# Kernel tuning notes

Hardware: AMD Instinct MI355X
Metric: run time of the kernel (lower is better)

Reference implementation:

```python
import jax, jax.numpy as jnp
import numpy as np

DIM = 1024
HEADS = 16

def setup_inputs() -> dict:
    key = jax.random.key(0)
    ks = jax.random.split(key, 5)
    x = jax.random.normal(ks[0], (4, 2048, DIM), dtype=jnp.float32)
    s = 1.0 / np.sqrt(DIM)
    Wqkv = jax.random.normal(ks[1], (DIM, 3 * DIM), dtype=jnp.float32) * s
    bqkv = jnp.zeros((3 * DIM,), dtype=jnp.float32)
    Wproj = jax.random.normal(ks[2], (DIM, DIM), dtype=jnp.float32) * s
    bproj = jnp.zeros((DIM,), dtype=jnp.float32)
    return {"x": x, "Wqkv": Wqkv, "bqkv": bqkv, "Wproj": Wproj, "bproj": bproj}

def reference(x, Wqkv, bqkv, Wproj, bproj):
    B, N, D = x.shape
    H = HEADS
    hd = D // H
    scale = hd ** (-0.5)
    qkv = x @ Wqkv + bqkv                      # [B, N, 3D]
    q, k, v = jnp.split(qkv, 3, axis=-1)
    # [B, N, H, hd] -> [B, H, N, hd]
    q = q.reshape(B, N, H, hd).transpose(0, 2, 1, 3)
    k = k.reshape(B, N, H, hd).transpose(0, 2, 1, 3)
    v = v.reshape(B, N, H, hd).transpose(0, 2, 1, 3)
    attn = jnp.einsum('bhqd,bhkd->bhqk', q, k) * scale
    attn = jax.nn.softmax(attn, axis=-1)
    out = jnp.einsum('bhqk,bhkd->bhqd', attn, v)
    out = out.transpose(0, 2, 1, 3).reshape(B, N, D)
    return out @ Wproj + bproj
```

## Files before the change

### kernel.cpp

```cpp
#include <hip/hip_runtime.h>
#include <hip/hip_bf16.h>
#include <math.h>


typedef __bf16 bf16;
typedef __bf16 bf16x4 __attribute__((ext_vector_type(4)));
typedef __bf16 bf16x8 __attribute__((ext_vector_type(8)));
typedef float f32x4 __attribute__((ext_vector_type(4)));

#define AS1(p) ((const __attribute__((address_space(1))) void*)(p))
#define AS3(p) ((__attribute__((address_space(3))) void*)(p))

__device__ __forceinline__ void async16(const void* g, void* l) {
    __builtin_amdgcn_global_load_lds(AS1(g), AS3(l), 16, 0, 0);
}

#if __has_builtin(__builtin_amdgcn_exp2f)
#define EXP2(x) __builtin_amdgcn_exp2f(x)
#else
#define EXP2(x) exp2f(x)
#endif

#define QSCALE 0.18033688011112042f


__global__ void cvt_f32_bf16(const float* __restrict__ in, bf16* __restrict__ out, int n4) {
    int i = blockIdx.x * blockDim.x + threadIdx.x;
    if (i < n4) {
        float4 v = ((const float4*)in)[i];
        bf16x4 o;
        o.x = (bf16)v.x; o.y = (bf16)v.y; o.z = (bf16)v.z; o.w = (bf16)v.w;
        ((bf16x4*)out)[i] = o;
    }
}

__global__ void transpose_cvt(const float* __restrict__ in, bf16* __restrict__ out, int K, int N) {
    __shared__ float t[32][33];
    const int n0 = blockIdx.x * 32, k0 = blockIdx.y * 32;
    const int tx = threadIdx.x, ty = threadIdx.y;
    #pragma unroll
    for (int j = 0; j < 32; j += 8)
        t[ty + j][tx] = in[(size_t)(k0 + ty + j) * N + n0 + tx];
    __syncthreads();
    #pragma unroll
    for (int j = 0; j < 32; j += 8)
        out[(size_t)(n0 + ty + j) * K + k0 + tx] = (bf16)t[tx][ty + j];
}


#define GEMM_STAGE(B) do { \
    async16(ga0, la0_##B); async16(ga1, la1_##B); \
    async16(gb0, lb0_##B); async16(gb1, lb1_##B); \
    ga0 += 32; ga1 += 32; gb0 += 32; gb1 += 32; \
} while (0)

#define GEMM_COMPUTE(B) do { \
    bf16x8 af[4], bfr[4]; \
    _Pragma("unroll") \
    for (int i = 0; i < 4; i++) \
        af[i] = *(const bf16x8*)(As##B + (wm + i * 16 + c) * 32 + quad * 8); \
    _Pragma("unroll") \
    for (int j = 0; j < 4; j++) \
        bfr[j] = *(const bf16x8*)(Bs##B + (wn + j * 16 + c) * 32 + quad * 8); \
    _Pragma("unroll") \
    for (int i = 0; i < 4; i++) \
        _Pragma("unroll") \
        for (int j = 0; j < 4; j++) \
            acc[i][j] = __builtin_amdgcn_mfma_f32_16x16x32_bf16(af[i], bfr[j], acc[i][j], 0, 0, 0); \
} while (0)

__device__ __forceinline__ void gemm_mainloop(const bf16* __restrict__ A,
                                              const bf16* __restrict__ Bt,
                                              int K, int m0, int n0,
                                              bf16* As0, bf16* As1,
                                              bf16* Bs0, bf16* Bs1, f32x4 acc[4][4]) {
    const int tid = threadIdx.x;
    const int wave = tid >> 6, lane = tid & 63;
    const int c = lane & 15, quad = lane >> 4;
    const int wm = (wave & 1) * 64, wn = (wave >> 1) * 64;

    const int ci0 = (wave * 2 + 0) * 64 + lane;
    const int ci1 = (wave * 2 + 1) * 64 + lane;
    const bf16* ga0 = A  + (size_t)(m0 + (ci0 >> 2)) * K + (ci0 & 3) * 8;
    const bf16* ga1 = A  + (size_t)(m0 + (ci1 >> 2)) * K + (ci1 & 3) * 8;
    const bf16* gb0 = Bt + (size_t)(n0 + (ci0 >> 2)) * K + (ci0 & 3) * 8;
    const bf16* gb1 = Bt + (size_t)(n0 + (ci1 >> 2)) * K + (ci1 & 3) * 8;
    bf16* la0_0 = As0 + (wave * 2 + 0) * 512;
    bf16* la1_0 = As0 + (wave * 2 + 1) * 512;
    bf16* la0_1 = As1 + (wave * 2 + 0) * 512;
    bf16* la1_1 = As1 + (wave * 2 + 1) * 512;
    bf16* lb0_0 = Bs0 + (wave * 2 + 0) * 512;
    bf16* lb1_0 = Bs0 + (wave * 2 + 1) * 512;
    bf16* lb0_1 = Bs1 + (wave * 2 + 0) * 512;
    bf16* lb1_1 = Bs1 + (wave * 2 + 1) * 512;

    const int nIter = K >> 6;
    GEMM_STAGE(0);
    __syncthreads();
    for (int t = 0; t < nIter; t++) {
        GEMM_STAGE(1);
        GEMM_COMPUTE(0);
        __syncthreads();
        if (t < nIter - 1) GEMM_STAGE(0);
        GEMM_COMPUTE(1);
        __syncthreads();
    }
}


__global__ __launch_bounds__(256) void gemm_qkv(const bf16* __restrict__ A,
                                                const bf16* __restrict__ Bt,
                                                const float* __restrict__ bias,
                                                bf16* __restrict__ Qb,
                                                bf16* __restrict__ Kb,
                                                bf16* __restrict__ Vtb) {
    __shared__ __align__(16) bf16 As0[128 * 32];
    __shared__ __align__(16) bf16 As1[128 * 32];
    __shared__ __align__(16) bf16 Bs0[128 * 32];
    __shared__ __align__(16) bf16 Bs1[128 * 32];
    f32x4 acc[4][4] = {};
    const int m0 = blockIdx.x * 128, n0 = blockIdx.y * 128;
    gemm_mainloop(A, Bt, 1024, m0, n0, As0, As1, Bs0, Bs1, acc);

    const int tid = threadIdx.x;
    const int wave = tid >> 6, lane = tid & 63;
    const int c = lane & 15, quad = lane >> 4;
    const int wm = (wave & 1) * 64, wn = (wave >> 1) * 64;
    const int sel = n0 >> 10;
    bf16* QK = (sel == 0) ? Qb : Kb;
    const float qs = (sel == 0) ? QSCALE : 1.0f;

    #pragma unroll
    for (int j = 0; j < 4; j++) {
        const int nfull = n0 + wn + j * 16 + c;
        const int nmod = nfull & 1023;
        const int h = nmod >> 6, e = nmod & 63;
        const float bv = bias[nfull];
        #pragma unroll
        for (int i = 0; i < 4; i++) {
            const int mbase = m0 + wm + i * 16 + quad * 4;
            const int b = mbase >> 11, t = mbase & 2047;
            if (sel < 2) {
                bf16* dst = QK + (((size_t)(b * 16 + h) * 2048 + t) * 64 + e);
                #pragma unroll
                for (int r = 0; r < 4; r++)
                    dst[(size_t)r * 64] = (bf16)((acc[i][j][r] + bv) * qs);
            } else {
                bf16* dst = Vtb + ((size_t)(b * 16 + h) * 64 + e) * 2048 + t;
                bf16x4 v;
                v.x = (bf16)(acc[i][j][0] + bv);
                v.y = (bf16)(acc[i][j][1] + bv);
                v.z = (bf16)(acc[i][j][2] + bv);
                v.w = (bf16)(acc[i][j][3] + bv);
                *(bf16x4*)dst = v;
            }
        }
    }
}


#define ATTN_STAGE(B) do { \
    async16(kS0, kD0_##B); async16(kS1, kD1_##B); \
    async16(vS0, vD0_##B); async16(vS1, vD1_##B); \
    kS0 += 4096; kS1 += 4096; vS0 += 64; vS1 += 64; \
} while (0)

#define ATTN_COMPUTE(B) do { \
    _Pragma("unroll") \
    for (int j = 0; j < 4; j++) { \
        bf16x8 kf0 = *(const bf16x8*)(kb0_##B + j * 1024); \
        bf16x8 kf1 = *(const bf16x8*)(kb1_##B + j * 1024); \
        f32x4 s0 = {}, s1 = {}; \
        __builtin_amdgcn_s_setprio(1); \
        s0 = __builtin_amdgcn_mfma_f32_16x16x32_bf16(kf0, qf[0][0], s0, 0, 0, 0); \
        s0 = __builtin_amdgcn_mfma_f32_16x16x32_bf16(kf1, qf[0][1], s0, 0, 0, 0); \
        s1 = __builtin_amdgcn_mfma_f32_16x16x32_bf16(kf0, qf[1][0], s1, 0, 0, 0); \
        s1 = __builtin_amdgcn_mfma_f32_16x16x32_bf16(kf1, qf[1][1], s1, 0, 0, 0); \
        __builtin_amdgcn_s_setprio(0); \
        _Pragma("unroll") \
        for (int r = 0; r < 4; r++) { s0[r] = EXP2(s0[r]); s1[r] = EXP2(s1[r]); } \
        lsum[0] += s0; \
        lsum[1] += s1; \
        bf16x4 p0, p1; \
        p0.x = (bf16)s0[0]; p0.y = (bf16)s0[1]; p0.z = (bf16)s0[2]; p0.w = (bf16)s0[3]; \
        p1.x = (bf16)s1[0]; p1.y = (bf16)s1[1]; p1.z = (bf16)s1[2]; p1.w = (bf16)s1[3]; \
        *(bf16x4*)(pwa + j * 16) = p0; \
        *(bf16x4*)(pwb + j * 16) = p1; \
    } \
    _Pragma("unroll") \
    for (int gks = 0; gks < 2; gks++) { \
        const bf16* vbg = gks ? vb1_##B : vb0_##B; \
        bf16x8 vf[4]; \
        _Pragma("unroll") \
        for (int n2 = 0; n2 < 4; n2++) \
            vf[n2] = *(const bf16x8*)(vbg + n2 * 1024); \
        bf16x8 pf0 = *(const bf16x8*)(pra + gks * 32); \
        bf16x8 pf1 = *(const bf16x8*)(prb + gks * 32); \
        __builtin_amdgcn_s_setprio(1); \
        _Pragma("unroll") \
        for (int n2 = 0; n2 < 4; n2++) { \
            o[0][n2] = __builtin_amdgcn_mfma_f32_16x16x32_bf16(pf0, vf[n2], o[0][n2], 0, 0, 0); \
            o[1][n2] = __builtin_amdgcn_mfma_f32_16x16x32_bf16(pf1, vf[n2], o[1][n2], 0, 0, 0); \
        } \
        __builtin_amdgcn_s_setprio(0); \
    } \
} while (0)

__global__ __launch_bounds__(256, 3) void attn_kernel(const bf16* __restrict__ Q,
                                                      const bf16* __restrict__ Kg,
                                                      const bf16* __restrict__ Vt,
                                                      bf16* __restrict__ Out) {
    __shared__ __align__(16) bf16 Ks0[64 * 64];
    __shared__ __align__(16) bf16 Ks1[64 * 64];
    __shared__ __align__(16) bf16 Vs0[64 * 64];
    __shared__ __align__(16) bf16 Vs1[64 * 64];
    __shared__ __align__(16) bf16 Pl[4 * 2 * 16 * 72];

    const int bh = blockIdx.x, qt = blockIdx.y;
    const int tid = threadIdx.x;
    const int wave = tid >> 6, lane = tid & 63;
    const int c = lane & 15, quad = lane >> 4;

    const bf16* Qb = Q + (size_t)bh * 2048 * 64;
    bf16* pw = Pl + wave * 2304;

    const int qbase = qt * 128 + wave * 32;

    bf16x8 qf[2][2];
    #pragma unroll
    for (int i = 0; i < 2; i++)
        #pragma unroll
        for (int ks = 0; ks < 2; ks++)
            qf[i][ks] = *(const bf16x8*)(Qb + (size_t)(qbase + i * 16 + c) * 64 + ks * 32 + quad * 8);

    const int s0i = tid, s1i = 256 + tid;
    const int rk0 = s0i >> 3, cg0 = (s0i & 7) ^ (rk0 & 7);
    const int rk1 = s1i >> 3, cg1 = (s1i & 7) ^ (rk1 & 7);
    const bf16* kS0 = Kg + (size_t)bh * 2048 * 64 + rk0 * 64 + cg0 * 8;
    const bf16* kS1 = Kg + (size_t)bh * 2048 * 64 + rk1 * 64 + cg1 * 8;
    const bf16* vS0 = Vt + (size_t)bh * 64 * 2048 + (size_t)rk0 * 2048 + cg0 * 8;
    const bf16* vS1 = Vt + (size_t)bh * 64 * 2048 + (size_t)rk1 * 2048 + cg1 * 8;
    bf16* kD0_0 = Ks0 + (size_t)(wave * 64) * 8;
    bf16* kD1_0 = Ks0 + (size_t)(256 + wave * 64) * 8;
    bf16* kD0_1 = Ks1 + (size_t)(wave * 64) * 8;
    bf16* kD1_1 = Ks1 + (size_t)(256 + wave * 64) * 8;
    bf16* vD0_0 = Vs0 + (size_t)(wave * 64) * 8;
    bf16* vD1_0 = Vs0 + (size_t)(256 + wave * 64) * 8;
    bf16* vD0_1 = Vs1 + (size_t)(wave * 64) * 8;
    bf16* vD1_1 = Vs1 + (size_t)(256 + wave * 64) * 8;

    const int sw = c & 7;
    const int ch0 = (quad ^ sw) * 8, ch1 = ((quad ^ sw) ^ 4) * 8;
    const bf16* kb0_0 = Ks0 + c * 64 + ch0;
    const bf16* kb1_0 = Ks0 + c * 64 + ch1;
    const bf16* kb0_1 = Ks1 + c * 64 + ch0;
    const bf16* kb1_1 = Ks1 + c * 64 + ch1;
    const bf16* vb0_0 = Vs0 + c * 64 + ch0;
    const bf16* vb1_0 = Vs0 + c * 64 + ch1;
    const bf16* vb0_1 = Vs1 + c * 64 + ch0;
    const bf16* vb1_1 = Vs1 + c * 64 + ch1;
    bf16* pwa = pw + c * 72 + quad * 4;
    bf16* pwb = pwa + 16 * 72;
    const bf16* pra = pw + c * 72 + quad * 8;
    const bf16* prb = pra + 16 * 72;

    f32x4 lsum[2] = {};
    f32x4 o[2][4] = {};

    ATTN_STAGE(0);
    __syncthreads();
    for (int kv2 = 0; kv2 < 16; kv2++) {
        ATTN_STAGE(1);
        ATTN_COMPUTE(0);
        __syncthreads();
        if (kv2 < 15) ATTN_STAGE(0);
        ATTN_COMPUTE(1);
        __syncthreads();
    }

    const int b = bh >> 4, hh = bh & 15;
    #pragma unroll
    for (int i = 0; i < 2; i++) {
        float lh = (lsum[i][0] + lsum[i][1]) + (lsum[i][2] + lsum[i][3]);
        lh += __shfl_xor(lh, 16);
        lh += __shfl_xor(lh, 32);
        const float li0 = __shfl(lh, quad * 4 + 0);
        const float li1 = __shfl(lh, quad * 4 + 1);
        const float li2 = __shfl(lh, quad * 4 + 2);
        const float li3 = __shfl(lh, quad * 4 + 3);
        const float inv[4] = {1.f / li0, 1.f / li1, 1.f / li2, 1.f / li3};
        #pragma unroll
        for (int r = 0; r < 4; r++) {
            const int token = b * 2048 + qbase + i * 16 + quad * 4 + r;
            #pragma unroll
            for (int n2 = 0; n2 < 4; n2++) {
                const int feat = hh * 64 + n2 * 16 + c;
                Out[(size_t)token * 1024 + feat] = (bf16)(o[i][n2][r] * inv[r]);
            }
        }
    }
}


__global__ __launch_bounds__(256) void gemm_proj(const bf16* __restrict__ A,
                                                 const bf16* __restrict__ Bt,
                                                 const float* __restrict__ bias,
                                                 float* __restrict__ Out) {
    __shared__ __align__(16) bf16 As0[128 * 32];
    __shared__ __align__(16) bf16 As1[128 * 32];
    __shared__ __align__(16) bf16 Bs0[128 * 32];
    __shared__ __align__(16) bf16 Bs1[128 * 32];
    f32x4 acc[4][4] = {};
    const int m0 = blockIdx.x * 128, n0 = blockIdx.y * 128;
    gemm_mainloop(A, Bt, 1024, m0, n0, As0, As1, Bs0, Bs1, acc);

    const int tid = threadIdx.x;
    const int wave = tid >> 6, lane = tid & 63;
    const int c = lane & 15, quad = lane >> 4;
    const int wm = (wave & 1) * 64, wn = (wave >> 1) * 64;

    #pragma unroll
    for (int j = 0; j < 4; j++) {
        const int nn = n0 + wn + j * 16 + c;
        const float bv = bias[nn];
        #pragma unroll
        for (int i = 0; i < 4; i++) {
            const int m = m0 + wm + i * 16 + quad * 4;
            #pragma unroll
            for (int r = 0; r < 4; r++)
                Out[(size_t)(m + r) * 1024 + nn] = acc[i][j][r] + bv;
        }
    }
}


extern "C" void kernel_launch(void* const* d_in, const int* in_sizes, int n_in,
                              void* d_out, int out_size, void* d_ws, size_t ws_size,
                              hipStream_t stream) {
    const float* x     = (const float*)d_in[0];
    const float* Wqkv  = (const float*)d_in[1];
    const float* bqkv  = (const float*)d_in[2];
    const float* Wproj = (const float*)d_in[3];
    const float* bproj = (const float*)d_in[4];
    float* out = (float*)d_out;

    char* ws = (char*)d_ws;
    bf16* xb     = (bf16*)(ws);
    bf16* wqkvt  = (bf16*)(ws + 16777216);
    bf16* wprojt = (bf16*)(ws + 23068672);
    bf16* Qb     = (bf16*)(ws + 25165824);
    bf16* Kb     = (bf16*)(ws + 41943040);
    bf16* Vtb    = (bf16*)(ws + 58720256);
    bf16* attno  = xb;

    cvt_f32_bf16<<<8192, 256, 0, stream>>>(x, xb, 2097152);
    transpose_cvt<<<dim3(96, 32), dim3(32, 8), 0, stream>>>(Wqkv, wqkvt, 1024, 3072);
    transpose_cvt<<<dim3(32, 32), dim3(32, 8), 0, stream>>>(Wproj, wprojt, 1024, 1024);
    gemm_qkv<<<dim3(64, 24), 256, 0, stream>>>(xb, wqkvt, bqkv, Qb, Kb, Vtb);
    attn_kernel<<<dim3(64, 16), 256, 0, stream>>>(Qb, Kb, Vtb, attno);
    gemm_proj<<<dim3(64, 8), 256, 0, stream>>>(attno, wprojt, bproj, out);
}
```

Measured before the change: 272.6 us.

## Enlarge GEMM block tile to 128x256 with 512 threads

```diff
diff --git a/kernel.cpp b/kernel.cpp
--- a/kernel.cpp
+++ b/kernel.cpp
@@ -49,9 +49,9 @@
 
 
 #define GEMM_STAGE(B) do { \
-    async16(ga0, la0_##B); async16(ga1, la1_##B); \
+    async16(ga0, la0_##B); \
     async16(gb0, lb0_##B); async16(gb1, lb1_##B); \
-    ga0 += 32; ga1 += 32; gb0 += 32; gb1 += 32; \
+    ga0 += 32; gb0 += 32; gb1 += 32; \
 } while (0)
 
 #define GEMM_COMPUTE(B) do { \
@@ -77,22 +77,17 @@
     const int tid = threadIdx.x;
     const int wave = tid >> 6, lane = tid & 63;
     const int c = lane & 15, quad = lane >> 4;
-    const int wm = (wave & 1) * 64, wn = (wave >> 1) * 64;
-
-    const int ci0 = (wave * 2 + 0) * 64 + lane;
-    const int ci1 = (wave * 2 + 1) * 64 + lane;
-    const bf16* ga0 = A  + (size_t)(m0 + (ci0 >> 2)) * K + (ci0 & 3) * 8;
-    const bf16* ga1 = A  + (size_t)(m0 + (ci1 >> 2)) * K + (ci1 & 3) * 8;
-    const bf16* gb0 = Bt + (size_t)(n0 + (ci0 >> 2)) * K + (ci0 & 3) * 8;
-    const bf16* gb1 = Bt + (size_t)(n0 + (ci1 >> 2)) * K + (ci1 & 3) * 8;
-    bf16* la0_0 = As0 + (wave * 2 + 0) * 512;
-    bf16* la1_0 = As0 + (wave * 2 + 1) * 512;
-    bf16* la0_1 = As1 + (wave * 2 + 0) * 512;
-    bf16* la1_1 = As1 + (wave * 2 + 1) * 512;
-    bf16* lb0_0 = Bs0 + (wave * 2 + 0) * 512;
-    bf16* lb1_0 = Bs0 + (wave * 2 + 1) * 512;
-    bf16* lb0_1 = Bs1 + (wave * 2 + 0) * 512;
-    bf16* lb1_1 = Bs1 + (wave * 2 + 1) * 512;
+    const int wm = (wave >> 2) * 64, wn = (wave & 3) * 64;
+
+    const bf16* ga0 = A  + (size_t)(m0 + (tid >> 2)) * K + (tid & 3) * 8;
+    const bf16* gb0 = Bt + (size_t)(n0 + (tid >> 2)) * K + (tid & 3) * 8;
+    const bf16* gb1 = Bt + (size_t)(n0 + 128 + (tid >> 2)) * K + (tid & 3) * 8;
+    bf16* la0_0 = As0 + wave * 512;
+    bf16* la0_1 = As1 + wave * 512;
+    bf16* lb0_0 = Bs0 + wave * 512;
+    bf16* lb0_1 = Bs1 + wave * 512;
+    bf16* lb1_0 = Bs0 + 4096 + wave * 512;
+    bf16* lb1_1 = Bs1 + 4096 + wave * 512;
 
     const int nIter = K >> 6;
     GEMM_STAGE(0);
@@ -108,24 +103,24 @@
 }
 
 
-__global__ __launch_bounds__(256) void gemm_qkv(const bf16* __restrict__ A,
-                                                const bf16* __restrict__ Bt,
-                                                const float* __restrict__ bias,
-                                                bf16* __restrict__ Qb,
-                                                bf16* __restrict__ Kb,
-                                                bf16* __restrict__ Vtb) {
+__global__ __launch_bounds__(512, 4) void gemm_qkv(const bf16* __restrict__ A,
+                                                   const bf16* __restrict__ Bt,
+                                                   const float* __restrict__ bias,
+                                                   bf16* __restrict__ Qb,
+                                                   bf16* __restrict__ Kb,
+                                                   bf16* __restrict__ Vtb) {
     __shared__ __align__(16) bf16 As0[128 * 32];
     __shared__ __align__(16) bf16 As1[128 * 32];
-    __shared__ __align__(16) bf16 Bs0[128 * 32];
-    __shared__ __align__(16) bf16 Bs1[128 * 32];
+    __shared__ __align__(16) bf16 Bs0[256 * 32];
+    __shared__ __align__(16) bf16 Bs1[256 * 32];
     f32x4 acc[4][4] = {};
-    const int m0 = blockIdx.x * 128, n0 = blockIdx.y * 128;
+    const int m0 = blockIdx.x * 128, n0 = blockIdx.y * 256;
     gemm_mainloop(A, Bt, 1024, m0, n0, As0, As1, Bs0, Bs1, acc);
 
     const int tid = threadIdx.x;
     const int wave = tid >> 6, lane = tid & 63;
     const int c = lane & 15, quad = lane >> 4;
-    const int wm = (wave & 1) * 64, wn = (wave >> 1) * 64;
+    const int wm = (wave >> 2) * 64, wn = (wave & 3) * 64;
     const int sel = n0 >> 10;
     bf16* QK = (sel == 0) ? Qb : Kb;
     const float qs = (sel == 0) ? QSCALE : 1.0f;
@@ -302,22 +297,22 @@
 }
 
 
-__global__ __launch_bounds__(256) void gemm_proj(const bf16* __restrict__ A,
-                                                 const bf16* __restrict__ Bt,
-                                                 const float* __restrict__ bias,
-                                                 float* __restrict__ Out) {
+__global__ __launch_bounds__(512, 4) void gemm_proj(const bf16* __restrict__ A,
+                                                    const bf16* __restrict__ Bt,
+                                                    const float* __restrict__ bias,
+                                                    float* __restrict__ Out) {
     __shared__ __align__(16) bf16 As0[128 * 32];
     __shared__ __align__(16) bf16 As1[128 * 32];
-    __shared__ __align__(16) bf16 Bs0[128 * 32];
-    __shared__ __align__(16) bf16 Bs1[128 * 32];
+    __shared__ __align__(16) bf16 Bs0[256 * 32];
+    __shared__ __align__(16) bf16 Bs1[256 * 32];
     f32x4 acc[4][4] = {};
-    const int m0 = blockIdx.x * 128, n0 = blockIdx.y * 128;
+    const int m0 = blockIdx.x * 128, n0 = blockIdx.y * 256;
     gemm_mainloop(A, Bt, 1024, m0, n0, As0, As1, Bs0, Bs1, acc);
 
     const int tid = threadIdx.x;
     const int wave = tid >> 6, lane = tid & 63;
     const int c = lane & 15, quad = lane >> 4;
-    const int wm = (wave & 1) * 64, wn = (wave >> 1) * 64;
+    const int wm = (wave >> 2) * 64, wn = (wave & 3) * 64;
 
     #pragma unroll
     for (int j = 0; j < 4; j++) {
@@ -356,7 +351,7 @@
     cvt_f32_bf16<<<8192, 256, 0, stream>>>(x, xb, 2097152);
     transpose_cvt<<<dim3(96, 32), dim3(32, 8), 0, stream>>>(Wqkv, wqkvt, 1024, 3072);
     transpose_cvt<<<dim3(32, 32), dim3(32, 8), 0, stream>>>(Wproj, wprojt, 1024, 1024);
-    gemm_qkv<<<dim3(64, 24), 256, 0, stream>>>(xb, wqkvt, bqkv, Qb, Kb, Vtb);
+    gemm_qkv<<<dim3(64, 12), 512, 0, stream>>>(xb, wqkvt, bqkv, Qb, Kb, Vtb);
     attn_kernel<<<dim3(64, 16), 256, 0, stream>>>(Qb, Kb, Vtb, attno);
-    gemm_proj<<<dim3(64, 8), 256, 0, stream>>>(attno, wprojt, bproj, out);
-}
+    gemm_proj<<<dim3(64, 4), 512, 0, stream>>>(attno, wprojt, bproj, out);
+}
```

Measured after the change: 281.0 us. 1.03x slower.
